# Kernel tuning notes

Hardware: AMD Instinct MI355X
Metric: run time of the kernel (lower is better)

## Reference

```python
import jax, jax.numpy as jnp
import numpy as np

# Dims (match init_kwargs / input_specs)
B, N, DIM, HEADS, DHEAD, CHUNK = 1, 2048, 1024, 8, 128, 64
HID = 4 * DHEAD            # MemoryMLP expansion_factor=4.0
DI = HEADS * DHEAD         # dim_inner
EPS = 1e-6
MAX_LR = 1.0               # default_step_transform_max_lr


def rmsnorm(x, w):
    return x * jax.lax.rsqrt(jnp.mean(jnp.square(x), -1, keepdims=True) + EPS) * w


def mem_forward(w0, w1, g, x):
    # ResidualNorm(MemoryMLP): y = RMSNorm(gelu(x@w0)@w1)*g + x
    h = jax.nn.gelu(x @ w0, approximate=False) @ w1
    return rmsnorm(h, g) + x


def setup_inputs() -> dict:
    key = jax.random.key(0)
    ks = jax.random.split(key, 12)
    s = lambda i, shape, sc: jax.random.normal(ks[i], shape, jnp.float32) * sc
    return dict(
        x=s(0, (B, N, DIM), 1.0),
        store_norm_w=jnp.ones((DIM,), jnp.float32),
        ret_norm_w=jnp.ones((DIM,), jnp.float32),
        Wq=s(1, (DIM, DI), DIM ** -0.5),
        Wk=s(2, (DIM, DI), DIM ** -0.5),
        Wv=s(3, (DIM, DI), DIM ** -0.5),
        W_step=s(4, (DIM, HEADS), DIM ** -0.5), b_step=jnp.zeros((HEADS,), jnp.float32),
        W_mom=s(5, (DIM, HEADS), DIM ** -0.5), b_mom=jnp.zeros((HEADS,), jnp.float32),
        W_decay=s(6, (DIM, HEADS), DIM ** -0.5), b_decay=jnp.zeros((HEADS,), jnp.float32),
        gate_W=s(7, (DIM, HEADS), DIM ** -0.5),
        combine_W=s(8, (DI, DIM), DI ** -0.5),
        mem_w0=s(9, (HEADS, DHEAD, HID), DHEAD ** -0.5),
        mem_w1=s(10, (HEADS, HID, DHEAD), HID ** -0.5),
        mem_g=jnp.ones((HEADS, DHEAD), jnp.float32),
    )


def reference(x, store_norm_w, ret_norm_w, Wq, Wk, Wv, W_step, b_step,
              W_mom, b_mom, W_decay, b_decay, gate_W, combine_W,
              mem_w0, mem_w1, mem_g):
    b, n, _ = x.shape
    nc = n // CHUNK
    BH = b * HEADS

    # ---- store path ----
    s = rmsnorm(x, store_norm_w)                                 # b n dim
    lr = jax.nn.sigmoid(s @ W_step + b_step) * MAX_LR            # b n h (per-token adaptive step)
    pooled = s.reshape(b, nc, CHUNK, DIM).mean(2)                # b nc dim (AveragePool chunk rep)
    mom = jax.nn.sigmoid(pooled @ W_mom + b_mom)                 # b nc h
    dec = jax.nn.sigmoid(pooled @ W_decay + b_decay)             # b nc h

    def to_chunks(t):  # b n (h d) -> (b h) nc c d
        return t.reshape(b, nc, CHUNK, HEADS, DHEAD).transpose(0, 3, 1, 2, 4).reshape(BH, nc, CHUNK, DHEAD)

    k = to_chunks(s @ Wk)
    v = to_chunks(s @ Wv)
    lr_c = lr.reshape(b, nc, CHUNK, HEADS).transpose(0, 3, 1, 2).reshape(BH, nc, CHUNK)
    mom_bh = mom.transpose(0, 2, 1).reshape(BH, nc)
    dec_bh = dec.transpose(0, 2, 1).reshape(BH, nc)

    # init fast weights per (b h)  (per_head_learned_parameters=True)
    w0 = jnp.broadcast_to(mem_w0[None], (b, HEADS, DHEAD, HID)).reshape(BH, DHEAD, HID)
    w1 = jnp.broadcast_to(mem_w1[None], (b, HEADS, HID, DHEAD)).reshape(BH, HID, DHEAD)
    g = jnp.broadcast_to(mem_g[None], (b, HEADS, DHEAD)).reshape(BH, DHEAD)

    def chunk_loss(w0_, w1_, g_, kc, vc, lrc):
        pred = mem_forward(w0_, w1_, g_, kc)                     # c d
        return jnp.sum(jnp.mean(jnp.square(pred - vc), -1) * lrc)

    grad_chunk = jax.grad(chunk_loss, argnums=(0, 1, 2))
    # vmap over chunks (same weights per chunk, per-sample grads), then over (b h)
    grads = jax.vmap(jax.vmap(grad_chunk, in_axes=(None, None, None, 0, 0, 0)))(w0, w1, g, k, v, lr_c)
    surprises = tuple(-gr for gr in grads)                       # each (BH, nc, ...)

    def combine(a, c):
        ga, xa = a
        gb, xb = c
        return (ga * gb, gb * xa + xb)

    def lin_scan(gates, xs):
        # y_i = gates_i * y_{i-1} + xs_i over chunk axis (axis=1)
        return jax.lax.associative_scan(combine, (gates, xs), axis=1)

    def expand(gates, ref):
        return gates.reshape(gates.shape + (1,) * (ref.ndim - 2))

    # momentum scan per parameter tensor
    updates = tuple(lin_scan(expand(mom_bh, su), su)[1] for su in surprises)

    # weight update scan: W_i = (1 - decay_i) * W_{i-1} + momentum_i, W_{-1} = init
    per_chunk_weights = []
    for upd, w_init in zip(updates, (w0, w1, g)):
        gates = expand(1.0 - dec_bh, upd)
        cumg, y = lin_scan(gates, upd)
        w_seq = y + cumg * w_init[:, None]                       # (BH, nc, ...)
        # retrieval at chunk i uses weights updated through chunk i-1
        per_chunk_weights.append(jnp.concatenate([w_init[:, None], w_seq[:, :-1]], axis=1))
    w0_c, w1_c, g_c = per_chunk_weights

    # ---- retrieve path ----
    r = rmsnorm(x, ret_norm_w)
    q = to_chunks(r @ Wq)                                        # (BH, nc, c, d)
    pred = jax.vmap(jax.vmap(mem_forward))(w0_c, w1_c, g_c, q)   # (BH, nc, c, d)
    out = pred.reshape(b, HEADS, n, DHEAD)                       # b h n d
    gate = jax.nn.sigmoid(r @ gate_W)                            # b n h (retrieve_gate, heads>1)
    out = out * gate.transpose(0, 2, 1)[..., None]
    out = out.transpose(0, 2, 1, 3).reshape(b, n, DI) @ combine_W
    return out
```

## Files before the change

kernel.cpp:

```cpp
#include <hip/hip_runtime.h>
#include <hip/hip_bf16.h>
#include <math.h>

#define NH   8
#define DHD  128
#define HIDN 512
#define CHK  64
#define NCH  32
#define MB   1048576ull

typedef unsigned short u16;
typedef unsigned int   u32;
typedef short s16x8 __attribute__((ext_vector_type(8)));
typedef float f32x4 __attribute__((ext_vector_type(4)));

#define MFMA(a,b,c) __builtin_amdgcn_mfma_f32_16x16x32_bf16((a),(b),(c),0,0,0)

__device__ __forceinline__ float bf2f(u16 v){ return __uint_as_float(((u32)v) << 16); }
__device__ __forceinline__ u16 f2bf(float f){
  u32 u = __float_as_uint(f);
  u += 0x7fffu + ((u >> 16) & 1u);
  return (u16)(u >> 16);
}
__device__ __forceinline__ u32 pack2(float a, float b){
  return (u32)f2bf(a) | ((u32)f2bf(b) << 16);
}
__device__ __forceinline__ float dot2(u32 a, u32 b){
  return __uint_as_float(a << 16)*__uint_as_float(b << 16)
       + __uint_as_float(a & 0xffff0000u)*__uint_as_float(b & 0xffff0000u);
}
__device__ __forceinline__ float waveRedSum(float v){
  #pragma unroll
  for (int off = 32; off; off >>= 1) v += __shfl_xor(v, off);
  return v;
}
__device__ __forceinline__ void gload16(const void* g, void* l){
  __builtin_amdgcn_global_load_lds(
      (const __attribute__((address_space(1))) u32*)g,
      (__attribute__((address_space(3))) u32*)l, 16, 0, 0);
}
__device__ __forceinline__ int swzb(int row, int colb){ return colb ^ ((row & 7) << 4); }
__device__ __forceinline__ int swza(int row, int colb){
  return colb ^ ((row & 7) << 4) ^ (((row >> 3) & 3) << 5);
}



__global__ __launch_bounds__(256) void k_rmsnorm(const float* __restrict__ x,
    const float* __restrict__ wst, const float* __restrict__ wrt,
    u16* __restrict__ s_bf, u16* __restrict__ r_bf){
  int row = blockIdx.x, t = threadIdx.x;
  float4 v = ((const float4*)(x + (size_t)row*1024))[t];
  float ss = v.x*v.x + v.y*v.y + v.z*v.z + v.w*v.w;
  ss = waveRedSum(ss);
  __shared__ float red[4];
  int wv = t >> 6, ln = t & 63;
  if (ln == 0) red[wv] = ss;
  __syncthreads();
  float rr = rsqrtf((red[0]+red[1]+red[2]+red[3])*(1.f/1024.f) + 1e-6f);
  float4 a = ((const float4*)wst)[t];
  float4 b = ((const float4*)wrt)[t];
  uint2 so = make_uint2(pack2(v.x*rr*a.x, v.y*rr*a.y), pack2(v.z*rr*a.z, v.w*rr*a.w));
  uint2 ro = make_uint2(pack2(v.x*rr*b.x, v.y*rr*b.y), pack2(v.z*rr*b.z, v.w*rr*b.w));
  *(uint2*)(s_bf + (size_t)row*1024 + t*4) = so;
  *(uint2*)(r_bf + (size_t)row*1024 + t*4) = ro;
}

__global__ __launch_bounds__(256) void k_pool(const u16* __restrict__ s_bf, float* __restrict__ pooled){
  int c = blockIdx.x; int d = blockIdx.y*256 + threadIdx.x;
  float acc = 0.f;
  for (int tt = 0; tt < 64; ++tt) acc += bf2f(s_bf[((size_t)c*64+tt)*1024 + d]);
  pooled[(size_t)c*1024 + d] = acc * (1.f/64.f);
}

__global__ __launch_bounds__(256) void k_lrgate(const u16* __restrict__ s_bf, const u16* __restrict__ r_bf,
    const u16* __restrict__ WsgL, const float* __restrict__ bstep,
    float* __restrict__ lrc, float* __restrict__ gate){
  int wv = threadIdx.x >> 6, ln = threadIdx.x & 63;
  int tok = blockIdx.x*4 + wv;
  const u16* sp = s_bf + (size_t)tok*1024 + ln*16;
  const u16* rp = r_bf + (size_t)tok*1024 + ln*16;
  uint4 s0 = *(const uint4*)sp, s1 = *(const uint4*)(sp+8);
  uint4 r0 = *(const uint4*)rp, r1 = *(const uint4*)(rp+8);
  #pragma unroll 4
  for (int o = 0; o < 16; ++o){
    const u16* wp = WsgL + (size_t)o*1024 + ln*16;
    uint4 w0v = *(const uint4*)wp, w1v = *(const uint4*)(wp+8);
    uint4 a0 = (o < 8) ? s0 : r0, a1 = (o < 8) ? s1 : r1;
    float acc = dot2(a0.x,w0v.x)+dot2(a0.y,w0v.y)+dot2(a0.z,w0v.z)+dot2(a0.w,w0v.w)
              + dot2(a1.x,w1v.x)+dot2(a1.y,w1v.y)+dot2(a1.z,w1v.z)+dot2(a1.w,w1v.w);
    acc = waveRedSum(acc);
    if (ln == 0){
      int h = o & 7;
      if (o < 8){
        float v = 1.f/(1.f+expf(-(acc + bstep[h])));
        lrc[((size_t)h*NCH + (tok>>6))*CHK + (tok&63)] = v;
      } else {
        gate[(size_t)tok*8 + h] = 1.f/(1.f+expf(-acc));
      }
    }
  }
}

__global__ __launch_bounds__(64) void k_momdec(const float* __restrict__ pooled,
    const float* __restrict__ Wmom, const float* __restrict__ bmom,
    const float* __restrict__ Wdec, const float* __restrict__ bdec,
    float* __restrict__ momb, float* __restrict__ decb){
  int c = blockIdx.x, ln = threadIdx.x;
  const float* prow = pooled + (size_t)c*1024;
  for (int o = 0; o < 16; ++o){
    int h = o & 7;
    const float* W = (o < 8) ? Wmom : Wdec;
    float acc = 0.f;
    for (int k = ln; k < 1024; k += 64) acc += prow[k]*W[(size_t)k*8+h];
    acc = waveRedSum(acc);
    if (ln == 0){
      float bb = (o < 8) ? bmom[h] : bdec[h];
      float v = 1.f/(1.f+expf(-(acc+bb)));
      if (o < 8) momb[h*NCH + c] = v; else decb[h*NCH + c] = v;
    }
  }
}

__global__ __launch_bounds__(256) void k_trf4(
    const float* __restrict__ A0, const float* __restrict__ A1,
    const float* __restrict__ A2, const float* __restrict__ A3,
    u16* __restrict__ O0, u16* __restrict__ O1, u16* __restrict__ O2, u16* __restrict__ O3){
  __shared__ u16 tile[32][34];
  int z = blockIdx.z;
  const float* in = (z==0)?A0:(z==1)?A1:(z==2)?A2:A3;
  u16* out = (z==0)?O0:(z==1)?O1:(z==2)?O2:O3;
  int c0 = blockIdx.x*32, r0 = blockIdx.y*32;
  int tx = threadIdx.x & 31, ty = threadIdx.x >> 5;
  #pragma unroll
  for (int k = 0; k < 4; ++k) tile[ty+k*8][tx] = f2bf(in[(size_t)(r0+ty+k*8)*1024 + c0+tx]);
  __syncthreads();
  #pragma unroll
  for (int k = 0; k < 4; ++k) out[(size_t)(c0+ty+k*8)*1024 + r0+tx] = tile[tx][ty+k*8];
}

__global__ __launch_bounds__(256) void k_packw(const float* __restrict__ mw0, const float* __restrict__ mw1,
    const float* __restrict__ Wstep, const float* __restrict__ gateW,
    u16* __restrict__ w0L, u16* __restrict__ w1L, u16* __restrict__ w1bL, u16* __restrict__ WsgL){
  int h = blockIdx.z, which = blockIdx.y;
  int i = blockIdx.x*256 + threadIdx.x;
  if (which == 3){
    if (h == 0 && i < 16384){
      int o = i >> 10, k = i & 1023;
      float v = (o < 8) ? Wstep[(size_t)k*8 + o] : gateW[(size_t)k*8 + (o-8)];
      WsgL[i] = f2bf(v);
    }
    return;
  }
  int r = i & 511, blk = i >> 9;
  int lg = r >> 7, lr = (r >> 3) & 15, e = r & 7;
  float v; u16* dst;
  if (which == 0){ int n0 = blk >> 2, ks = blk & 3; int hid = n0*16+lr, d = ks*32+lg*8+e;
    v = mw0[(size_t)h*65536 + (size_t)d*512 + hid]; dst = w0L; }
  else if (which == 1){ int n0 = blk >> 4, ks = blk & 15; int d = n0*16+lr, hid = ks*32+lg*8+e;
    v = mw1[(size_t)h*65536 + (size_t)hid*128 + d]; dst = w1L; }
  else { int n0 = blk >> 2, ks = blk & 3; int hid = n0*16+lr, d = ks*32+lg*8+e;
    v = mw1[(size_t)h*65536 + (size_t)hid*128 + d]; dst = w1bL; }
  dst[(size_t)h*65536 + i] = f2bf(v);
}

__device__ __forceinline__ void gemm_body(const u16* __restrict__ A, const u16* __restrict__ BT,
    void* __restrict__ Cp, int mode){
  __shared__ char As[8192];
  __shared__ char Bs[16384];
  int t = threadIdx.x, l = t & 63, w = t >> 6, lr16 = l & 15, lg = l >> 4;
  int wm = w & 1, wn = w >> 1;
  int bm = blockIdx.x*64, bn = blockIdx.y*128;
  f32x4 acc[2][2];
  #pragma unroll
  for (int mt = 0; mt < 2; ++mt)
    #pragma unroll
    for (int nt = 0; nt < 2; ++nt) acc[mt][nt] = (f32x4){0.f,0.f,0.f,0.f};
  for (int k0 = 0; k0 < 1024; k0 += 64){
    gload16(A  + (size_t)(bm + (t>>3))*1024      + k0 + (t&7)*8, As + w*1024);
    gload16(BT + (size_t)(bn + (t>>3))*1024      + k0 + (t&7)*8, Bs + w*1024);
    gload16(BT + (size_t)(bn + 64 + (t>>3))*1024 + k0 + (t&7)*8, Bs + 8192 + w*1024);
    __syncthreads();
    #pragma unroll
    for (int ks = 0; ks < 2; ++ks){
      s16x8 xa[2], yb[2];
      #pragma unroll
      for (int mt = 0; mt < 2; ++mt){ int row = wm*32 + mt*16 + lr16;
        xa[mt] = *(const s16x8*)(As + row*128 + ks*64 + lg*16); }
      #pragma unroll
      for (int nt = 0; nt < 2; ++nt){ int row = wn*32 + nt*16 + lr16;
        yb[nt] = *(const s16x8*)(Bs + row*128 + ks*64 + lg*16); }
      #pragma unroll
      for (int mt = 0; mt < 2; ++mt)
        #pragma unroll
        for (int nt = 0; nt < 2; ++nt) acc[mt][nt] = MFMA(xa[mt], yb[nt], acc[mt][nt]);
    }
    __syncthreads();
  }
  #pragma unroll
  for (int mt = 0; mt < 2; ++mt)
    #pragma unroll
    for (int nt = 0; nt < 2; ++nt)
      #pragma unroll
      for (int j = 0; j < 4; ++j){
        int row = bm + wm*32 + mt*16 + lg*4 + j;
        int coln = bn + wn*32 + nt*16 + lr16;
        if (mode == 0) ((float*)Cp)[(size_t)row*1024 + coln] = acc[mt][nt][j];
        else { int cI = row>>6, tok = row&63, h = coln>>7, d = coln&127;
          ((u16*)Cp)[((size_t)(h*32+cI)*64 + tok)*128 + d] = f2bf(acc[mt][nt][j]); }
      }
}

__global__ __launch_bounds__(512) void k_gemm_bf(const u16* __restrict__ A, const u16* __restrict__ BT,
    void* __restrict__ Cp, int mode){ gemm_body(A, BT, Cp, mode); }

__global__ __launch_bounds__(512) void k_gemm3(
    const u16* __restrict__ s_bf, const u16* __restrict__ r_bf,
    const u16* __restrict__ WkT, const u16* __restrict__ WvT, const u16* __restrict__ WqT,
    u16* __restrict__ Kc, u16* __restrict__ Vc, u16* __restrict__ Qc){
  int z = blockIdx.z;
  const u16* A = (z==2) ? r_bf : s_bf;
  const u16* BT = (z==0) ? WkT : (z==1) ? WvT : WqT;
  u16* C = (z==0) ? Kc : (z==1) ? Vc : Qc;
  gemm_body(A, BT, (void*)C, 1);
}

__global__ __launch_bounds__(512, 4) void k_grad(
    const u16* __restrict__ Kc, const u16* __restrict__ Vc, const float* __restrict__ lrc,
    const u16* __restrict__ w0L, const u16* __restrict__ w1L, const u16* __restrict__ w1bL,
    const float* __restrict__ mg,
    u16* __restrict__ SW0, u16* __restrict__ SW1, float* __restrict__ SG, u16* __restrict__ dhg){
  extern __shared__ char sm[];
  char* a_s   = sm;
  char* dhT_s = sm + 65536;
  char* duT_s = a_s;
  char* kcT_s = dhT_s;
  float* scr  = (float*)dhT_s;

  int c = blockIdx.x, bh = blockIdx.y, t = threadIdx.x;
  size_t bc = (size_t)bh*NCH + c;
  int l = t & 63, w = t >> 6, lr16 = l & 15, lg = l >> 4;

  const u16* kc_g = Kc + bc*8192;
  const u16* vc_g = Vc + bc*8192;

  uint2 upr[16];
  const u16* w0Lh = w0L + (size_t)bh*65536;
  #pragma unroll
  for (int tgi = 0; tgi < 4; ++tgi){
    s16x8 xk[4];
    #pragma unroll
    for (int ks = 0; ks < 4; ++ks)
      xk[ks] = *(const s16x8*)(kc_g + (size_t)(tgi*16+lr16)*128 + ks*32 + lg*8);
    #pragma unroll
    for (int n0l = 0; n0l < 4; ++n0l){
      int n0 = w*4 + n0l;
      f32x4 acc = {0.f,0.f,0.f,0.f};
      const u16* yb = w0Lh + (size_t)n0*2048 + l*8;
      #pragma unroll
      for (int ks = 0; ks < 4; ++ks) acc = MFMA(xk[ks], *(const s16x8*)(yb + ks*512), acc);
      int hid = n0*16 + lr16;
      float upv[4];
      #pragma unroll
      for (int j = 0; j < 4; ++j){
        int tok = tgi*16 + lg*4 + j;
        float u = acc[j];
        float cdf = 0.5f*(1.f + erff(u*0.70710678118654752f));
        upv[j] = cdf + u*0.3989422804014327f*expf(-0.5f*u*u);
        *(u16*)(a_s + tok*1024 + swza(tok, hid*2)) = f2bf(u*cdf);
      }
      upr[tgi*4 + n0l] = make_uint2(pack2(upv[0], upv[1]), pack2(upv[2], upv[3]));
    }
  }
  __syncthreads();

  int tg = w & 3, dhf = w >> 2;
  int tokb = tg*16, tok0 = tokb + lg*4;
  const u16* w1Lh = w1L + (size_t)bh*65536;
  f32x4 hD[4];
  #pragma unroll
  for (int n0l = 0; n0l < 4; ++n0l){
    f32x4 acc = {0.f,0.f,0.f,0.f};
    const u16* yb = w1Lh + (size_t)(dhf*4 + n0l)*8192 + l*8;
    #pragma unroll
    for (int kb = 0; kb < 4; ++kb){
      s16x8 xa[4];
      #pragma unroll
      for (int kk = 0; kk < 4; ++kk){
        int k = kb*4 + kk, row = tokb + lr16;
        xa[kk] = *(const s16x8*)(a_s + row*1024 + swza(row, (k*32+lg*8)*2));
      }
      #pragma unroll
      for (int kk = 0; kk < 4; ++kk) acc = MFMA(xa[kk], *(const s16x8*)(yb + (kb*4+kk)*512), acc);
    }
    hD[n0l] = acc;
  }
  #pragma unroll
  for (int j = 0; j < 4; ++j){
    float s = 0.f;
    #pragma unroll
    for (int n0l = 0; n0l < 4; ++n0l) s += hD[n0l][j]*hD[n0l][j];
    s += __shfl_xor(s,1); s += __shfl_xor(s,2); s += __shfl_xor(s,4); s += __shfl_xor(s,8);
    if (lr16 == 0) scr[dhf*64 + tok0 + j] = s;
  }
  __syncthreads();
  float rv[4], lrv[4], dotp[4];
  #pragma unroll
  for (int j = 0; j < 4; ++j){
    int tok = tok0 + j;
    float tot = scr[tok] + scr[64 + tok];
    rv[j] = rsqrtf(tot*(1.f/128.f) + 1e-6f);
    lrv[j] = lrc[bc*64 + tok];
    dotp[j] = 0.f;
  }
  float dn[4][4];
  #pragma unroll
  for (int n0l = 0; n0l < 4; ++n0l){
    int d = dhf*64 + n0l*16 + lr16;
    float g0 = mg[(size_t)bh*128 + d];
    float dgav = 0.f;
    #pragma unroll
    for (int j = 0; j < 4; ++j){
      int tok = tok0 + j;
      float h = hD[n0l][j];
      float nrm = h*rv[j];
      float kcv = bf2f(kc_g[(size_t)tok*128 + d]);
      float vcv = bf2f(vc_g[(size_t)tok*128 + d]);
      float p = nrm*g0 + kcv;
      float dp = (2.f/128.f)*lrv[j]*(p - vcv);
      dgav += dp*nrm;
      float dnv = dp*g0;
      dn[n0l][j] = dnv;
      dotp[j] += dnv*h;
    }
    dgav += __shfl_xor(dgav,16); dgav += __shfl_xor(dgav,32);
    if (lg == 0) scr[256 + w*64 + n0l*16 + lr16] = dgav;
  }
  #pragma unroll
  for (int j = 0; j < 4; ++j){
    float dd = dotp[j];
    dd += __shfl_xor(dd,1); dd += __shfl_xor(dd,2); dd += __shfl_xor(dd,4); dd += __shfl_xor(dd,8);
    if (lr16 == 0) scr[128 + dhf*64 + tok0 + j] = dd;
  }
  __syncthreads();
  float dotv[4];
  #pragma unroll
  for (int j = 0; j < 4; ++j){
    int tok = tok0 + j;
    dotv[j] = scr[128 + tok] + scr[128 + 64 + tok];
  }
  if (t < 128){
    int dh2 = t >> 6, dl = t & 63;
    float s = scr[256 + (dh2*4+0)*64 + dl] + scr[256 + (dh2*4+1)*64 + dl]
            + scr[256 + (dh2*4+2)*64 + dl] + scr[256 + (dh2*4+3)*64 + dl];
    SG[bc*128 + t] = -s;
  }
  __syncthreads();
  #pragma unroll
  for (int n0l = 0; n0l < 4; ++n0l){
    int d = dhf*64 + n0l*16 + lr16;
    float dhv[4];
    #pragma unroll
    for (int j = 0; j < 4; ++j){
      int tok = tok0 + j;
      float c3 = rv[j]*rv[j]*rv[j]*(1.f/128.f);
      dhv[j] = rv[j]*dn[n0l][j] - c3*dotv[j]*hD[n0l][j];
      dhg[bc*8192 + (size_t)tok*128 + d] = f2bf(dhv[j]);
    }
    *(uint2*)(dhT_s + d*128 + swzb(d, tok0*2)) =
        make_uint2(pack2(dhv[0], dhv[1]), pack2(dhv[2], dhv[3]));
  }
  __syncthreads();

  {
    s16x8 yB[4][2];
    #pragma unroll
    for (int n0l = 0; n0l < 4; ++n0l){
      int hid = w*64 + n0l*16 + lr16;
      #pragma unroll
      for (int ks = 0; ks < 2; ++ks){
        s16x8 v;
        #pragma unroll
        for (int e = 0; e < 8; ++e){ int tok = ks*32 + lg*8 + e;
          v[e] = *(const short*)(a_s + tok*1024 + swza(tok, hid*2)); }
        yB[n0l][ks] = v;
      }
    }
    __syncthreads();
    u16* stg = (u16*)(a_s + w*8192);
    #pragma unroll 1
    for (int half = 0; half < 2; ++half){
      #pragma unroll
      for (int mt4 = 0; mt4 < 4; ++mt4){
        int mt = half*4 + mt4; int row = mt*16 + lr16;
        s16x8 xD0 = *(const s16x8*)(dhT_s + row*128 + swzb(row, (lg*8)*2));
        s16x8 xD1 = *(const s16x8*)(dhT_s + row*128 + swzb(row, (32+lg*8)*2));
        #pragma unroll
        for (int n0l = 0; n0l < 4; ++n0l){
          f32x4 acc = {0.f,0.f,0.f,0.f};
          acc = MFMA(xD0, yB[n0l][0], acc);
          acc = MFMA(xD1, yB[n0l][1], acc);
          int base = mt4*1024 + (n0l>>1)*512 + (((n0l*2)+(lr16>>3))&3)*128 + (lr16&7);
          #pragma unroll
          for (int j = 0; j < 4; ++j)
            stg[base + (lg*4+j)*8] = f2bf(-acc[j]);
        }
      }
      asm volatile("s_waitcnt lgkmcnt(0)" ::: "memory");
      #pragma unroll
      for (int mt4 = 0; mt4 < 4; ++mt4){
        int mt = half*4 + mt4;
        u16* gb = SW1 + bc*65536 + (size_t)(mt*16 + w*2)*512;
        s16x8 o0 = *(const s16x8*)(stg + mt4*1024 + l*16);
        s16x8 o1 = *(const s16x8*)(stg + mt4*1024 + l*16 + 8);
        *(s16x8*)(gb + l*16) = o0;
        *(s16x8*)(gb + l*16 + 8) = o1;
      }
    }
  }
  __syncthreads();

  #pragma unroll
  for (int i = 0; i < 2; ++i){
    int idx = i*512 + t;
    int tok = idx & 63, d0 = (idx >> 6)*8;
    s16x8 kv = *(const s16x8*)(kc_g + (size_t)tok*128 + d0);
    #pragma unroll
    for (int e = 0; e < 8; ++e)
      *(u16*)(kcT_s + (d0+e)*128 + swzb(d0+e, tok*2)) = kv[e];
  }
  {
    const u16* dhb = dhg + bc*8192;
    const u16* w1bh = w1bL + (size_t)bh*65536;
    #pragma unroll 1
    for (int mt = 0; mt < 4; ++mt){
      s16x8 xDh[4];
      #pragma unroll
      for (int ks = 0; ks < 4; ++ks)
        xDh[ks] = *(const s16x8*)(dhb + (size_t)(mt*16+lr16)*128 + ks*32 + lg*8);
      #pragma unroll
      for (int n0l = 0; n0l < 4; ++n0l){
        int hid = w*64 + n0l*16 + lr16;
        const u16* xb = w1bh + (size_t)(w*4 + n0l)*2048 + l*8;
        f32x4 acc = {0.f,0.f,0.f,0.f};
        #pragma unroll
        for (int ks = 0; ks < 4; ++ks) acc = MFMA(xDh[ks], *(const s16x8*)(xb + ks*512), acc);
        int tk0 = mt*16 + lg*4;
        uint2 ur = upr[mt*4 + n0l];
        float u0 = bf2f((u16)(ur.x & 0xffff)), u1 = bf2f((u16)(ur.x >> 16));
        float u2 = bf2f((u16)(ur.y & 0xffff)), u3 = bf2f((u16)(ur.y >> 16));
        *(uint2*)(duT_s + hid*128 + swzb(hid, tk0*2)) =
            make_uint2(pack2(acc[0]*u0, acc[1]*u1), pack2(acc[2]*u2, acc[3]*u3));
      }
    }
  }
  __syncthreads();

  {
    s16x8 yK[8][2];
    #pragma unroll
    for (int n0 = 0; n0 < 8; ++n0){
      int d = n0*16 + lr16;
      #pragma unroll
      for (int ks = 0; ks < 2; ++ks)
        yK[n0][ks] = *(const s16x8*)(kcT_s + d*128 + swzb(d, (ks*32+lg*8)*2));
    }
    #pragma unroll 1
    for (int mi = 0; mi < 4; ++mi){
      int hid = w*64 + mi*16 + lr16;
      s16x8 xU0 = *(const s16x8*)(duT_s + hid*128 + swzb(hid, (lg*8)*2));
      s16x8 xU1 = *(const s16x8*)(duT_s + hid*128 + swzb(hid, (32+lg*8)*2));
      u16* stgw = (u16*)(duT_s + (size_t)(w*64 + mi*16)*128);
      u16* gb = SW0 + bc*65536 + (size_t)(w*4 + mi)*2048;
      #pragma unroll 1
      for (int hh = 0; hh < 2; ++hh){
        #pragma unroll
        for (int n0h = 0; n0h < 4; ++n0h){
          int n0 = hh*4 + n0h;
          f32x4 acc = {0.f,0.f,0.f,0.f};
          acc = MFMA(xU0, yK[n0][0], acc);
          acc = MFMA(xU1, yK[n0][1], acc);
          int base = (n0h>>1)*512 + (((n0*2)+(lr16>>3))&3)*128 + (lr16&7);
          #pragma unroll
          for (int j = 0; j < 4; ++j)
            stgw[base + (lg*4+j)*8] = f2bf(-acc[j]);
        }
        asm volatile("s_waitcnt lgkmcnt(0)" ::: "memory");
        s16x8 o0 = *(const s16x8*)(stgw + l*16);
        s16x8 o1 = *(const s16x8*)(stgw + l*16 + 8);
        *(s16x8*)(gb + hh*1024 + l*16) = o0;
        *(s16x8*)(gb + hh*1024 + l*16 + 8) = o1;
      }
    }
  }
}

__global__ __launch_bounds__(256) void k_scan(
    const u16* __restrict__ w0L, const u16* __restrict__ w1L, const float* __restrict__ mg,
    const u16* __restrict__ SW0, const u16* __restrict__ SW1, const float* __restrict__ SG,
    const float* __restrict__ momb, const float* __restrict__ decb,
    u16* __restrict__ W0C, u16* __restrict__ W1C, float* __restrict__ GC){
  int bh = blockIdx.y;
  int e = blockIdx.x*256 + threadIdx.x;
  const float* momp = momb + bh*NCH;
  const float* decp = decb + bh*NCH;
  float m = 0.f, Wv;
  if (e < 65536){
    Wv = bf2f(w0L[(size_t)bh*65536 + e]);
    const u16* su = SW0 + (size_t)bh*NCH*65536 + e;
    u16* outp = W0C + (size_t)bh*NCH*65536 + e;
    for (int c = 0; c < NCH; ++c){
      outp[(size_t)c*65536] = f2bf(Wv);
      m = momp[c]*m + bf2f(su[(size_t)c*65536]);
      Wv = (1.f - decp[c])*Wv + m;
    }
  } else if (e < 131072){
    int e2 = e - 65536;
    Wv = bf2f(w1L[(size_t)bh*65536 + e2]);
    const u16* su = SW1 + (size_t)bh*NCH*65536 + e2;
    u16* outp = W1C + (size_t)bh*NCH*65536 + e2;
    for (int c = 0; c < NCH; ++c){
      outp[(size_t)c*65536] = f2bf(Wv);
      m = momp[c]*m + bf2f(su[(size_t)c*65536]);
      Wv = (1.f - decp[c])*Wv + m;
    }
  } else if (e < 131200){
    int e3 = e - 131072;
    Wv = mg[(size_t)bh*128 + e3];
    const float* su = SG + (size_t)bh*NCH*128 + e3;
    float* outp = GC + (size_t)bh*NCH*128 + e3;
    for (int c = 0; c < NCH; ++c){
      outp[(size_t)c*128] = Wv;
      m = momp[c]*m + su[(size_t)c*128];
      Wv = (1.f - decp[c])*Wv + m;
    }
  }
}

__global__ __launch_bounds__(512) void k_retr(
    const u16* __restrict__ Qc, const u16* __restrict__ W0C, const u16* __restrict__ W1C,
    const float* __restrict__ GC, const float* __restrict__ gate, u16* __restrict__ OH){
  extern __shared__ char sm[];
  char* a_s = sm;
  float* scr = (float*)(sm + 65536);
  int c = blockIdx.x, bh = blockIdx.y, t = threadIdx.x;
  size_t bc = (size_t)bh*NCH + c;
  int l = t & 63, w = t >> 6, lr16 = l & 15, lg = l >> 4;
  int tg = w & 3, dhf = w >> 2;
  const u16* q_g = Qc + bc*8192;

  s16x8 xq[4];
  #pragma unroll
  for (int k = 0; k < 4; ++k)
    xq[k] = *(const s16x8*)(q_g + (size_t)(tg*16+lr16)*128 + k*32 + lg*8);
  const u16* w0c = W0C + bc*65536;
  for (int n0h = 0; n0h < 16; ++n0h){
    int n0 = dhf*16 + n0h;
    f32x4 acc = {0.f,0.f,0.f,0.f};
    const u16* yb = w0c + (size_t)n0*2048 + l*8;
    #pragma unroll
    for (int k = 0; k < 4; ++k) acc = MFMA(xq[k], *(const s16x8*)(yb + k*512), acc);
    int hid = n0*16 + lr16;
    #pragma unroll
    for (int j = 0; j < 4; ++j){
      int tok = tg*16 + lg*4 + j;
      float u = acc[j];
      float av = u*0.5f*(1.f + erff(u*0.70710678118654752f));
      *(u16*)(a_s + tok*1024 + swza(tok, hid*2)) = f2bf(av);
    }
  }
  __syncthreads();
  s16x8 xa[16];
  #pragma unroll
  for (int k = 0; k < 16; ++k){ int row = tg*16 + lr16;
    xa[k] = *(const s16x8*)(a_s + row*1024 + swza(row, (k*32+lg*8)*2)); }
  const u16* w1c = W1C + bc*65536;
  f32x4 hD[4];
  #pragma unroll
  for (int n0l = 0; n0l < 4; ++n0l){
    f32x4 acc = {0.f,0.f,0.f,0.f};
    const u16* yb = w1c + (size_t)(dhf*4 + n0l)*8192 + l*8;
    #pragma unroll
    for (int k = 0; k < 16; ++k) acc = MFMA(xa[k], *(const s16x8*)(yb + k*512), acc);
    hD[n0l] = acc;
  }
  #pragma unroll
  for (int j = 0; j < 4; ++j){
    float s = 0.f;
    #pragma unroll
    for (int n0l = 0; n0l < 4; ++n0l) s += hD[n0l][j]*hD[n0l][j];
    s += __shfl_xor(s,1); s += __shfl_xor(s,2); s += __shfl_xor(s,4); s += __shfl_xor(s,8);
    if (lr16 == 0) scr[dhf*64 + tg*16 + lg*4 + j] = s;
  }
  __syncthreads();
  float rv[4], gtv[4];
  #pragma unroll
  for (int j = 0; j < 4; ++j){
    int tok = tg*16 + lg*4 + j;
    rv[j] = rsqrtf((scr[tok] + scr[64 + tok])*(1.f/128.f) + 1e-6f);
    gtv[j] = gate[(size_t)(c*64 + tok)*8 + bh];
  }
  #pragma unroll
  for (int n0l = 0; n0l < 4; ++n0l){
    int d = dhf*64 + n0l*16 + lr16;
    float g0 = GC[bc*128 + d];
    #pragma unroll
    for (int j = 0; j < 4; ++j){
      int tok = tg*16 + lg*4 + j; int tokg = c*64 + tok;
      float qv = bf2f(q_g[(size_t)tok*128 + d]);
      float p = hD[n0l][j]*rv[j]*g0 + qv;
      OH[(size_t)tokg*1024 + bh*128 + d] = f2bf(p*gtv[j]);
    }
  }
}

extern "C" void kernel_launch(void* const* d_in, const int* in_sizes, int n_in,
                              void* d_out, int out_size, void* d_ws, size_t ws_size,
                              hipStream_t stream) {
  (void)in_sizes; (void)n_in; (void)out_size; (void)ws_size;
  const float* x     = (const float*)d_in[0];
  const float* snw   = (const float*)d_in[1];
  const float* rnw   = (const float*)d_in[2];
  const float* Wq    = (const float*)d_in[3];
  const float* Wk    = (const float*)d_in[4];
  const float* Wv    = (const float*)d_in[5];
  const float* Wstep = (const float*)d_in[6];
  const float* bstep = (const float*)d_in[7];
  const float* Wmom  = (const float*)d_in[8];
  const float* bmom  = (const float*)d_in[9];
  const float* Wdec  = (const float*)d_in[10];
  const float* bdec  = (const float*)d_in[11];
  const float* gateW = (const float*)d_in[12];
  const float* combW = (const float*)d_in[13];
  const float* mw0   = (const float*)d_in[14];
  const float* mw1   = (const float*)d_in[15];
  const float* mg    = (const float*)d_in[16];
  float* out = (float*)d_out;

  char* Wb = (char*)d_ws;
  u16* Qc    = (u16*)(Wb + 0*MB);
  u16* Kc    = (u16*)(Wb + 4*MB);
  u16* Vc    = (u16*)(Wb + 8*MB);
  u16* s_bf  = (u16*)(Wb + 12*MB);
  u16* r_bf  = (u16*)(Wb + 16*MB);
  u16* WqT   = (u16*)(Wb + 20*MB);
  u16* WkT   = (u16*)(Wb + 22*MB);
  u16* WvT   = (u16*)(Wb + 24*MB);
  u16* combT = (u16*)(Wb + 26*MB);
  u16* w0L   = (u16*)(Wb + 28*MB);
  u16* w1L   = (u16*)(Wb + 29*MB);
  u16* w1bL  = (u16*)(Wb + 30*MB);
  u16* OH    = (u16*)(Wb + 31*MB);
  u16* SW0   = (u16*)(Wb + 35*MB);
  u16* SW1   = (u16*)(Wb + 67*MB);
  u16* W0C   = (u16*)(Wb + 99*MB);
  u16* W1C   = (u16*)(Wb + 131*MB);
  float* pooled = (float*)(Wb + 163*MB);
  float* lrc    = (float*)(Wb + 163*MB + 131072);
  float* momb   = (float*)(Wb + 163*MB + 196608);
  float* decb   = (float*)(Wb + 163*MB + 197632);
  float* gate   = (float*)(Wb + 163*MB + 198656);
  float* SG     = (float*)(Wb + 163*MB + 264192);
  float* GC     = (float*)(Wb + 163*MB + 395264);
  u16* WsgL  = (u16*)(Wb + 163*MB + 526336);
  u16* dhg   = (u16*)(Wb + 164*MB);

  hipFuncSetAttribute((const void*)k_grad, hipFuncAttributeMaxDynamicSharedMemorySize, 81920);
  hipFuncSetAttribute((const void*)k_retr, hipFuncAttributeMaxDynamicSharedMemorySize, 66560);

  k_rmsnorm<<<2048, 256, 0, stream>>>(x, snw, rnw, s_bf, r_bf);
  k_pool<<<dim3(32,4), 256, 0, stream>>>(s_bf, pooled);
  k_packw<<<dim3(256,4,8), 256, 0, stream>>>(mw0, mw1, Wstep, gateW, w0L, w1L, w1bL, WsgL);
  k_lrgate<<<512, 256, 0, stream>>>(s_bf, r_bf, WsgL, bstep, lrc, gate);
  k_momdec<<<32, 64, 0, stream>>>(pooled, Wmom, bmom, Wdec, bdec, momb, decb);
  k_trf4<<<dim3(32,32,4), 256, 0, stream>>>(Wq, Wk, Wv, combW, WqT, WkT, WvT, combT);
  k_gemm3<<<dim3(32,8,3), 512, 0, stream>>>(s_bf, r_bf, WkT, WvT, WqT, Kc, Vc, Qc);
  k_grad<<<dim3(32,8), 512, 81920, stream>>>(Kc, Vc, lrc, w0L, w1L, w1bL, mg, SW0, SW1, SG, dhg);
  k_scan<<<dim3(513,8), 256, 0, stream>>>(w0L, w1L, mg, SW0, SW1, SG, momb, decb, W0C, W1C, GC);
  k_retr<<<dim3(32,8), 512, 66560, stream>>>(Qc, W0C, W1C, GC, gate, OH);
  k_gemm_bf<<<dim3(32,8), 512, 0, stream>>>(OH, combT, (void*)out, 0);
}
```

Before: 259.7 us.

## Split gradient kernel into two kernels with doubled grid parallelism

The single per-chunk gradient kernel (256 blocks) becomes two kernels of 512 blocks each. gradA splits tokens into halves and writes activations, gelu derivatives, dh and partial g-gradients to global memory. gradB splits the hidden dimension into halves and computes the SW0/SW1 outer products from those buffers. This is meant to fill the GPU's compute units better and reduce LDS per block, at the cost of an extra launch and extra global traffic for the intermediates (about 16MB each way for a_g and upTg).

```diff
diff --git a/kernel.cpp b/kernel.cpp
--- a/kernel.cpp
+++ b/kernel.cpp
@@ -40,6 +40,7 @@
       (__attribute__((address_space(3))) u32*)l, 16, 0, 0);
 }
 __device__ __forceinline__ int swzb(int row, int colb){ return colb ^ ((row & 7) << 4); }
+__device__ __forceinline__ int swz64(int row, int colb){ return colb ^ ((row & 3) << 4); }
 __device__ __forceinline__ int swza(int row, int colb){
   return colb ^ ((row & 7) << 4) ^ (((row >> 3) & 3) << 5);
 }
@@ -225,29 +226,30 @@
   gemm_body(A, BT, (void*)C, 1);
 }
 
-__global__ __launch_bounds__(512, 4) void k_grad(
+__global__ __launch_bounds__(512, 4) void k_gradA(
     const u16* __restrict__ Kc, const u16* __restrict__ Vc, const float* __restrict__ lrc,
-    const u16* __restrict__ w0L, const u16* __restrict__ w1L, const u16* __restrict__ w1bL,
-    const float* __restrict__ mg,
-    u16* __restrict__ SW0, u16* __restrict__ SW1, float* __restrict__ SG, u16* __restrict__ dhg){
+    const u16* __restrict__ w0L, const u16* __restrict__ w1L, const float* __restrict__ mg,
+    u16* __restrict__ a_g, u16* __restrict__ upTg, u16* __restrict__ dhg, float* __restrict__ SGp){
   extern __shared__ char sm[];
-  char* a_s   = sm;
-  char* dhT_s = sm + 65536;
-  char* duT_s = a_s;
-  char* kcT_s = dhT_s;
-  float* scr  = (float*)dhT_s;
-
-  int c = blockIdx.x, bh = blockIdx.y, t = threadIdx.x;
+  char* a_s  = sm;
+  char* dhst = sm + 32768;
+  float* scr = (float*)(sm + 40960);
+  char* upst = a_s;
+
+  int bx = blockIdx.x;
+  int c = bx >> 1, th = bx & 1;
+  int bh = blockIdx.y, t = threadIdx.x;
   size_t bc = (size_t)bh*NCH + c;
+  int T0 = th*32;
   int l = t & 63, w = t >> 6, lr16 = l & 15, lg = l >> 4;
 
-  const u16* kc_g = Kc + bc*8192;
-  const u16* vc_g = Vc + bc*8192;
-
-  uint2 upr[16];
+  const u16* kc_g = Kc + bc*8192 + (size_t)T0*128;
+  const u16* vc_g = Vc + bc*8192 + (size_t)T0*128;
+
+  uint2 upr[8];
   const u16* w0Lh = w0L + (size_t)bh*65536;
   #pragma unroll
-  for (int tgi = 0; tgi < 4; ++tgi){
+  for (int tgi = 0; tgi < 2; ++tgi){
     s16x8 xk[4];
     #pragma unroll
     for (int ks = 0; ks < 4; ++ks)
@@ -260,10 +262,11 @@
       #pragma unroll
       for (int ks = 0; ks < 4; ++ks) acc = MFMA(xk[ks], *(const s16x8*)(yb + ks*512), acc);
       int hid = n0*16 + lr16;
+      int tk0 = tgi*16 + lg*4;
       float upv[4];
       #pragma unroll
       for (int j = 0; j < 4; ++j){
-        int tok = tgi*16 + lg*4 + j;
+        int tok = tk0 + j;
         float u = acc[j];
         float cdf = 0.5f*(1.f + erff(u*0.70710678118654752f));
         upv[j] = cdf + u*0.3989422804014327f*expf(-0.5f*u*u);
@@ -274,49 +277,50 @@
   }
   __syncthreads();
 
-  int tg = w & 3, dhf = w >> 2;
+  #pragma unroll
+  for (int i = 0; i < 4; ++i){
+    int idx = i*512 + t;
+    int tok = idx >> 6, seg = idx & 63;
+    s16x8 v = *(const s16x8*)(a_s + tok*1024 + swza(tok, seg*16));
+    *(s16x8*)(a_g + bc*32768 + (size_t)(T0+tok)*512 + seg*8) = v;
+  }
+
+  int tg = w & 1, hq = w >> 1;
   int tokb = tg*16, tok0 = tokb + lg*4;
+  s16x8 xa[16];
+  #pragma unroll
+  for (int k = 0; k < 16; ++k){ int row = tokb + lr16;
+    xa[k] = *(const s16x8*)(a_s + row*1024 + swza(row, (k*32+lg*8)*2)); }
   const u16* w1Lh = w1L + (size_t)bh*65536;
-  f32x4 hD[4];
-  #pragma unroll
-  for (int n0l = 0; n0l < 4; ++n0l){
+  f32x4 hD[2];
+  #pragma unroll
+  for (int n0l = 0; n0l < 2; ++n0l){
     f32x4 acc = {0.f,0.f,0.f,0.f};
-    const u16* yb = w1Lh + (size_t)(dhf*4 + n0l)*8192 + l*8;
-    #pragma unroll
-    for (int kb = 0; kb < 4; ++kb){
-      s16x8 xa[4];
-      #pragma unroll
-      for (int kk = 0; kk < 4; ++kk){
-        int k = kb*4 + kk, row = tokb + lr16;
-        xa[kk] = *(const s16x8*)(a_s + row*1024 + swza(row, (k*32+lg*8)*2));
-      }
-      #pragma unroll
-      for (int kk = 0; kk < 4; ++kk) acc = MFMA(xa[kk], *(const s16x8*)(yb + (kb*4+kk)*512), acc);
-    }
+    const u16* yb = w1Lh + (size_t)(hq*2 + n0l)*8192 + l*8;
+    #pragma unroll
+    for (int k = 0; k < 16; ++k) acc = MFMA(xa[k], *(const s16x8*)(yb + k*512), acc);
     hD[n0l] = acc;
   }
   #pragma unroll
   for (int j = 0; j < 4; ++j){
-    float s = 0.f;
-    #pragma unroll
-    for (int n0l = 0; n0l < 4; ++n0l) s += hD[n0l][j]*hD[n0l][j];
+    float s = hD[0][j]*hD[0][j] + hD[1][j]*hD[1][j];
     s += __shfl_xor(s,1); s += __shfl_xor(s,2); s += __shfl_xor(s,4); s += __shfl_xor(s,8);
-    if (lr16 == 0) scr[dhf*64 + tok0 + j] = s;
+    if (lr16 == 0) scr[hq*32 + tok0 + j] = s;
   }
   __syncthreads();
   float rv[4], lrv[4], dotp[4];
   #pragma unroll
   for (int j = 0; j < 4; ++j){
     int tok = tok0 + j;
-    float tot = scr[tok] + scr[64 + tok];
+    float tot = scr[tok] + scr[32+tok] + scr[64+tok] + scr[96+tok];
     rv[j] = rsqrtf(tot*(1.f/128.f) + 1e-6f);
-    lrv[j] = lrc[bc*64 + tok];
+    lrv[j] = lrc[bc*64 + T0 + tok];
     dotp[j] = 0.f;
   }
-  float dn[4][4];
-  #pragma unroll
-  for (int n0l = 0; n0l < 4; ++n0l){
-    int d = dhf*64 + n0l*16 + lr16;
+  float dn[2][4];
+  #pragma unroll
+  for (int n0l = 0; n0l < 2; ++n0l){
+    int d = hq*32 + n0l*16 + lr16;
     float g0 = mg[(size_t)bh*128 + d];
     float dgav = 0.f;
     #pragma unroll
@@ -334,88 +338,125 @@
       dotp[j] += dnv*h;
     }
     dgav += __shfl_xor(dgav,16); dgav += __shfl_xor(dgav,32);
-    if (lg == 0) scr[256 + w*64 + n0l*16 + lr16] = dgav;
+    if (lg == 0) scr[256 + tg*128 + d] = dgav;
   }
   #pragma unroll
   for (int j = 0; j < 4; ++j){
     float dd = dotp[j];
     dd += __shfl_xor(dd,1); dd += __shfl_xor(dd,2); dd += __shfl_xor(dd,4); dd += __shfl_xor(dd,8);
-    if (lr16 == 0) scr[128 + dhf*64 + tok0 + j] = dd;
+    if (lr16 == 0) scr[128 + hq*32 + tok0 + j] = dd;
   }
   __syncthreads();
   float dotv[4];
   #pragma unroll
   for (int j = 0; j < 4; ++j){
     int tok = tok0 + j;
-    dotv[j] = scr[128 + tok] + scr[128 + 64 + tok];
-  }
-  if (t < 128){
-    int dh2 = t >> 6, dl = t & 63;
-    float s = scr[256 + (dh2*4+0)*64 + dl] + scr[256 + (dh2*4+1)*64 + dl]
-            + scr[256 + (dh2*4+2)*64 + dl] + scr[256 + (dh2*4+3)*64 + dl];
-    SG[bc*128 + t] = -s;
-  }
-  __syncthreads();
-  #pragma unroll
-  for (int n0l = 0; n0l < 4; ++n0l){
-    int d = dhf*64 + n0l*16 + lr16;
-    float dhv[4];
+    dotv[j] = scr[128+tok] + scr[160+tok] + scr[192+tok] + scr[224+tok];
+  }
+  if (t < 128)
+    SGp[bc*256 + (size_t)th*128 + t] = -(scr[256+t] + scr[384+t]);
+  #pragma unroll
+  for (int n0l = 0; n0l < 2; ++n0l){
+    int d = hq*32 + n0l*16 + lr16;
     #pragma unroll
     for (int j = 0; j < 4; ++j){
       int tok = tok0 + j;
       float c3 = rv[j]*rv[j]*rv[j]*(1.f/128.f);
-      dhv[j] = rv[j]*dn[n0l][j] - c3*dotv[j]*hD[n0l][j];
-      dhg[bc*8192 + (size_t)tok*128 + d] = f2bf(dhv[j]);
-    }
-    *(uint2*)(dhT_s + d*128 + swzb(d, tok0*2)) =
-        make_uint2(pack2(dhv[0], dhv[1]), pack2(dhv[2], dhv[3]));
-  }
-  __syncthreads();
-
+      float dhv = rv[j]*dn[n0l][j] - c3*dotv[j]*hD[n0l][j];
+      *(u16*)(dhst + tok*256 + swzb(tok, d*2)) = f2bf(dhv);
+    }
+  }
+  __syncthreads();
   {
-    s16x8 yB[4][2];
+    int tok = t >> 4, seg = t & 15;
+    s16x8 v = *(const s16x8*)(dhst + tok*256 + swzb(tok, seg*16));
+    *(s16x8*)(dhg + bc*8192 + (size_t)(T0+tok)*128 + seg*8) = v;
+  }
+  #pragma unroll
+  for (int tgi = 0; tgi < 2; ++tgi)
     #pragma unroll
     for (int n0l = 0; n0l < 4; ++n0l){
-      int hid = w*64 + n0l*16 + lr16;
+      int hid = (w*4 + n0l)*16 + lr16;
+      int tk0 = tgi*16 + lg*4;
+      *(uint2*)(upst + hid*64 + swz64(hid, tk0*2)) = upr[tgi*4 + n0l];
+    }
+  __syncthreads();
+  #pragma unroll
+  for (int i = 0; i < 4; ++i){
+    int idx = i*512 + t;
+    int hid = idx >> 2, q = idx & 3;
+    s16x8 v = *(const s16x8*)(upst + hid*64 + swz64(hid, q*16));
+    *(s16x8*)(upTg + bc*32768 + (size_t)hid*64 + th*32 + q*8) = v;
+  }
+}
+
+__global__ __launch_bounds__(512, 4) void k_gradB(
+    const u16* __restrict__ Kc, const u16* __restrict__ dhg, const u16* __restrict__ a_g,
+    const u16* __restrict__ upTg, const u16* __restrict__ w1bL,
+    u16* __restrict__ SW0, u16* __restrict__ SW1){
+  extern __shared__ char sm[];
+  char* aH  = sm;
+  char* dhT = sm + 32768;
+  char* st1 = sm + 49152;
+  char* duT = aH;
+  char* kcT = dhT;
+  int bx = blockIdx.x;
+  int c = bx >> 1, hh = bx & 1;
+  int bh = blockIdx.y, t = threadIdx.x;
+  size_t bc = (size_t)bh*NCH + c;
+  int l = t & 63, w = t >> 6, lr16 = l & 15, lg = l >> 4;
+
+  #pragma unroll
+  for (int i = 0; i < 4; ++i){
+    int idx = i*512 + t;
+    int tok = idx >> 5, seg = idx & 31;
+    s16x8 v = *(const s16x8*)(a_g + bc*32768 + (size_t)tok*512 + hh*256 + seg*8);
+    *(s16x8*)(aH + tok*512 + swza(tok, seg*16)) = v;
+  }
+  #pragma unroll
+  for (int i = 0; i < 2; ++i){
+    int idx = i*512 + t;
+    int tok = idx & 63, d0 = (idx >> 6)*8;
+    s16x8 kv = *(const s16x8*)(dhg + bc*8192 + (size_t)tok*128 + d0);
+    #pragma unroll
+    for (int e = 0; e < 8; ++e)
+      *(u16*)(dhT + (d0+e)*128 + swzb(d0+e, tok*2)) = kv[e];
+  }
+  __syncthreads();
+
+  {
+    s16x8 yB[2][2];
+    #pragma unroll
+    for (int n0l = 0; n0l < 2; ++n0l){
+      int hidL = w*32 + n0l*16 + lr16;
       #pragma unroll
       for (int ks = 0; ks < 2; ++ks){
         s16x8 v;
         #pragma unroll
         for (int e = 0; e < 8; ++e){ int tok = ks*32 + lg*8 + e;
-          v[e] = *(const short*)(a_s + tok*1024 + swza(tok, hid*2)); }
+          v[e] = *(const short*)(aH + tok*512 + swza(tok, hidL*2)); }
         yB[n0l][ks] = v;
       }
     }
-    __syncthreads();
-    u16* stg = (u16*)(a_s + w*8192);
+    u16* stg = (u16*)(st1 + w*1024);
     #pragma unroll 1
-    for (int half = 0; half < 2; ++half){
-      #pragma unroll
-      for (int mt4 = 0; mt4 < 4; ++mt4){
-        int mt = half*4 + mt4; int row = mt*16 + lr16;
-        s16x8 xD0 = *(const s16x8*)(dhT_s + row*128 + swzb(row, (lg*8)*2));
-        s16x8 xD1 = *(const s16x8*)(dhT_s + row*128 + swzb(row, (32+lg*8)*2));
+    for (int mt = 0; mt < 8; ++mt){
+      int row = mt*16 + lr16;
+      s16x8 xD0 = *(const s16x8*)(dhT + row*128 + swzb(row, lg*16));
+      s16x8 xD1 = *(const s16x8*)(dhT + row*128 + swzb(row, 64 + lg*16));
+      #pragma unroll
+      for (int n0l = 0; n0l < 2; ++n0l){
+        f32x4 acc = {0.f,0.f,0.f,0.f};
+        acc = MFMA(xD0, yB[n0l][0], acc);
+        acc = MFMA(xD1, yB[n0l][1], acc);
+        int base = (n0l*2 + (lr16>>3))*128 + (lr16&7);
         #pragma unroll
-        for (int n0l = 0; n0l < 4; ++n0l){
-          f32x4 acc = {0.f,0.f,0.f,0.f};
-          acc = MFMA(xD0, yB[n0l][0], acc);
-          acc = MFMA(xD1, yB[n0l][1], acc);
-          int base = mt4*1024 + (n0l>>1)*512 + (((n0l*2)+(lr16>>3))&3)*128 + (lr16&7);
-          #pragma unroll
-          for (int j = 0; j < 4; ++j)
-            stg[base + (lg*4+j)*8] = f2bf(-acc[j]);
-        }
+        for (int j = 0; j < 4; ++j)
+          stg[base + (lg*4+j)*8] = f2bf(-acc[j]);
       }
       asm volatile("s_waitcnt lgkmcnt(0)" ::: "memory");
-      #pragma unroll
-      for (int mt4 = 0; mt4 < 4; ++mt4){
-        int mt = half*4 + mt4;
-        u16* gb = SW1 + bc*65536 + (size_t)(mt*16 + w*2)*512;
-        s16x8 o0 = *(const s16x8*)(stg + mt4*1024 + l*16);
-        s16x8 o1 = *(const s16x8*)(stg + mt4*1024 + l*16 + 8);
-        *(s16x8*)(gb + l*16) = o0;
-        *(s16x8*)(gb + l*16 + 8) = o1;
-      }
+      s16x8 o = *(const s16x8*)(stg + l*8);
+      *(s16x8*)(SW1 + bc*65536 + (size_t)(mt*16 + hh*8 + w)*512 + l*8) = o;
     }
   }
   __syncthreads();
@@ -424,10 +465,10 @@
   for (int i = 0; i < 2; ++i){
     int idx = i*512 + t;
     int tok = idx & 63, d0 = (idx >> 6)*8;
-    s16x8 kv = *(const s16x8*)(kc_g + (size_t)tok*128 + d0);
+    s16x8 kv = *(const s16x8*)(Kc + bc*8192 + (size_t)tok*128 + d0);
     #pragma unroll
     for (int e = 0; e < 8; ++e)
-      *(u16*)(kcT_s + (d0+e)*128 + swzb(d0+e, tok*2)) = kv[e];
+      *(u16*)(kcT + (d0+e)*128 + swzb(d0+e, tok*2)) = kv[e];
   }
   {
     const u16* dhb = dhg + bc*8192;
@@ -439,17 +480,19 @@
       for (int ks = 0; ks < 4; ++ks)
         xDh[ks] = *(const s16x8*)(dhb + (size_t)(mt*16+lr16)*128 + ks*32 + lg*8);
       #pragma unroll
-      for (int n0l = 0; n0l < 4; ++n0l){
-        int hid = w*64 + n0l*16 + lr16;
-        const u16* xb = w1bh + (size_t)(w*4 + n0l)*2048 + l*8;
+      for (int n0l = 0; n0l < 2; ++n0l){
+        int n0 = hh*16 + w*2 + n0l;
+        const u16* xb = w1bh + (size_t)n0*2048 + l*8;
         f32x4 acc = {0.f,0.f,0.f,0.f};
         #pragma unroll
         for (int ks = 0; ks < 4; ++ks) acc = MFMA(xDh[ks], *(const s16x8*)(xb + ks*512), acc);
+        int hidL = w*32 + n0l*16 + lr16;
+        int hid = hh*256 + hidL;
         int tk0 = mt*16 + lg*4;
-        uint2 ur = upr[mt*4 + n0l];
+        uint2 ur = *(const uint2*)(upTg + bc*32768 + (size_t)hid*64 + tk0);
         float u0 = bf2f((u16)(ur.x & 0xffff)), u1 = bf2f((u16)(ur.x >> 16));
         float u2 = bf2f((u16)(ur.y & 0xffff)), u3 = bf2f((u16)(ur.y >> 16));
-        *(uint2*)(duT_s + hid*128 + swzb(hid, tk0*2)) =
+        *(uint2*)(duT + hidL*128 + swzb(hidL, tk0*2)) =
             make_uint2(pack2(acc[0]*u0, acc[1]*u1), pack2(acc[2]*u2, acc[3]*u3));
       }
     }
@@ -459,28 +502,28 @@
   {
     s16x8 yK[8][2];
     #pragma unroll
-    for (int n0 = 0; n0 < 8; ++n0){
-      int d = n0*16 + lr16;
+    for (int nd = 0; nd < 8; ++nd){
+      int d = nd*16 + lr16;
       #pragma unroll
       for (int ks = 0; ks < 2; ++ks)
-        yK[n0][ks] = *(const s16x8*)(kcT_s + d*128 + swzb(d, (ks*32+lg*8)*2));
+        yK[nd][ks] = *(const s16x8*)(kcT + d*128 + swzb(d, (ks*32+lg*8)*2));
     }
     #pragma unroll 1
-    for (int mi = 0; mi < 4; ++mi){
-      int hid = w*64 + mi*16 + lr16;
-      s16x8 xU0 = *(const s16x8*)(duT_s + hid*128 + swzb(hid, (lg*8)*2));
-      s16x8 xU1 = *(const s16x8*)(duT_s + hid*128 + swzb(hid, (32+lg*8)*2));
-      u16* stgw = (u16*)(duT_s + (size_t)(w*64 + mi*16)*128);
-      u16* gb = SW0 + bc*65536 + (size_t)(w*4 + mi)*2048;
+    for (int mi = 0; mi < 2; ++mi){
+      int hidL = w*32 + mi*16 + lr16;
+      s16x8 xU0 = *(const s16x8*)(duT + hidL*128 + swzb(hidL, lg*16));
+      s16x8 xU1 = *(const s16x8*)(duT + hidL*128 + swzb(hidL, 64 + lg*16));
+      u16* stgw = (u16*)(duT + (size_t)(w*32 + mi*16)*128);
+      u16* gb = SW0 + bc*65536 + (size_t)(hh*16 + w*2 + mi)*2048;
       #pragma unroll 1
-      for (int hh = 0; hh < 2; ++hh){
+      for (int kh = 0; kh < 2; ++kh){
         #pragma unroll
         for (int n0h = 0; n0h < 4; ++n0h){
-          int n0 = hh*4 + n0h;
+          int nd = kh*4 + n0h;
           f32x4 acc = {0.f,0.f,0.f,0.f};
-          acc = MFMA(xU0, yK[n0][0], acc);
-          acc = MFMA(xU1, yK[n0][1], acc);
-          int base = (n0h>>1)*512 + (((n0*2)+(lr16>>3))&3)*128 + (lr16&7);
+          acc = MFMA(xU0, yK[nd][0], acc);
+          acc = MFMA(xU1, yK[nd][1], acc);
+          int base = (n0h>>1)*512 + (((n0h*2)+(lr16>>3))&3)*128 + (lr16&7);
           #pragma unroll
           for (int j = 0; j < 4; ++j)
             stgw[base + (lg*4+j)*8] = f2bf(-acc[j]);
@@ -488,8 +531,8 @@
         asm volatile("s_waitcnt lgkmcnt(0)" ::: "memory");
         s16x8 o0 = *(const s16x8*)(stgw + l*16);
         s16x8 o1 = *(const s16x8*)(stgw + l*16 + 8);
-        *(s16x8*)(gb + hh*1024 + l*16) = o0;
-        *(s16x8*)(gb + hh*1024 + l*16 + 8) = o1;
+        *(s16x8*)(gb + kh*1024 + l*16) = o0;
+        *(s16x8*)(gb + kh*1024 + l*16 + 8) = o1;
       }
     }
   }
@@ -497,7 +540,7 @@
 
 __global__ __launch_bounds__(256) void k_scan(
     const u16* __restrict__ w0L, const u16* __restrict__ w1L, const float* __restrict__ mg,
-    const u16* __restrict__ SW0, const u16* __restrict__ SW1, const float* __restrict__ SG,
+    const u16* __restrict__ SW0, const u16* __restrict__ SW1, const float* __restrict__ SGp,
     const float* __restrict__ momb, const float* __restrict__ decb,
     u16* __restrict__ W0C, u16* __restrict__ W1C, float* __restrict__ GC){
   int bh = blockIdx.y;
@@ -527,11 +570,12 @@
   } else if (e < 131200){
     int e3 = e - 131072;
     Wv = mg[(size_t)bh*128 + e3];
-    const float* su = SG + (size_t)bh*NCH*128 + e3;
+    const float* su = SGp + (size_t)bh*NCH*256 + e3;
     float* outp = GC + (size_t)bh*NCH*128 + e3;
     for (int c = 0; c < NCH; ++c){
       outp[(size_t)c*128] = Wv;
-      m = momp[c]*m + su[(size_t)c*128];
+      float sv = su[(size_t)c*256] + su[(size_t)c*256 + 128];
+      m = momp[c]*m + sv;
       Wv = (1.f - decp[c])*Wv + m;
     }
   }
@@ -660,13 +704,16 @@
   float* momb   = (float*)(Wb + 163*MB + 196608);
   float* decb   = (float*)(Wb + 163*MB + 197632);
   float* gate   = (float*)(Wb + 163*MB + 198656);
-  float* SG     = (float*)(Wb + 163*MB + 264192);
-  float* GC     = (float*)(Wb + 163*MB + 395264);
-  u16* WsgL  = (u16*)(Wb + 163*MB + 526336);
-  u16* dhg   = (u16*)(Wb + 164*MB);
-
-  hipFuncSetAttribute((const void*)k_grad, hipFuncAttributeMaxDynamicSharedMemorySize, 81920);
-  hipFuncSetAttribute((const void*)k_retr, hipFuncAttributeMaxDynamicSharedMemorySize, 66560);
+  float* GC     = (float*)(Wb + 163*MB + 264192);
+  u16* WsgL  = (u16*)(Wb + 163*MB + 395264);
+  u16* a_g   = (u16*)(Wb + 164*MB);
+  u16* upTg  = (u16*)(Wb + 180*MB);
+  u16* dhg   = (u16*)(Wb + 196*MB);
+  float* SGp = (float*)(Wb + 200*MB);
+
+  hipFuncSetAttribute((const void*)k_gradA, hipFuncAttributeMaxDynamicSharedMemorySize, 49152);
+  hipFuncSetAttribute((const void*)k_gradB, hipFuncAttributeMaxDynamicSharedMemorySize, 57344);
+  hipFuncSetAttribute((const void*)k_retr,  hipFuncAttributeMaxDynamicSharedMemorySize, 66560);
 
   k_rmsnorm<<<2048, 256, 0, stream>>>(x, snw, rnw, s_bf, r_bf);
   k_pool<<<dim3(32,4), 256, 0, stream>>>(s_bf, pooled);
@@ -675,8 +722,9 @@
   k_momdec<<<32, 64, 0, stream>>>(pooled, Wmom, bmom, Wdec, bdec, momb, decb);
   k_trf4<<<dim3(32,32,4), 256, 0, stream>>>(Wq, Wk, Wv, combW, WqT, WkT, WvT, combT);
   k_gemm3<<<dim3(32,8,3), 512, 0, stream>>>(s_bf, r_bf, WkT, WvT, WqT, Kc, Vc, Qc);
-  k_grad<<<dim3(32,8), 512, 81920, stream>>>(Kc, Vc, lrc, w0L, w1L, w1bL, mg, SW0, SW1, SG, dhg);
-  k_scan<<<dim3(513,8), 256, 0, stream>>>(w0L, w1L, mg, SW0, SW1, SG, momb, decb, W0C, W1C, GC);
+  k_gradA<<<dim3(64,8), 512, 49152, stream>>>(Kc, Vc, lrc, w0L, w1L, mg, a_g, upTg, dhg, SGp);
+  k_gradB<<<dim3(64,8), 512, 57344, stream>>>(Kc, dhg, a_g, upTg, w1bL, SW0, SW1);
+  k_scan<<<dim3(513,8), 256, 0, stream>>>(w0L, w1L, mg, SW0, SW1, SGp, momb, decb, W0C, W1C, GC);
   k_retr<<<dim3(32,8), 512, 66560, stream>>>(Qc, W0C, W1C, GC, gate, OH);
   k_gemm_bf<<<dim3(32,8), 512, 0, stream>>>(OH, combT, (void*)out, 0);
 }
```

After: 290.9 us. +12.0%, slower.
